# Kernel optimization log

Measured on AMD Instinct MI355X. Metric: run time of the kernel, lower is better.

Reference implementation:

```python
import jax, jax.numpy as jnp
from jax import lax
import numpy as np

B = 262144   # batch of independent series
K = 64       # forecast horizon (init k)
D_IN = 200   # Non_AR_net input dim (Linear(200,100))
H = 100      # hidden width


def setup_inputs() -> dict:
    key = jax.random.key(0)
    ks = jax.random.split(key, 10)
    f32 = jnp.float32
    x = jax.random.normal(ks[0], (B, D_IN), f32)
    last_mu = jax.random.normal(ks[1], (B,), f32)
    # last_sigma is the variance state; keep it strictly positive
    last_sigma = jax.random.uniform(ks[2], (B,), f32) + 0.5
    # MLP params (Kaiming-ish scale)
    W1 = jax.random.normal(ks[3], (D_IN, H), f32) / np.float32(np.sqrt(D_IN))
    b1 = jnp.zeros((H,), f32)
    W2 = jax.random.normal(ks[4], (H, H), f32) / np.float32(np.sqrt(H))
    b2 = jnp.zeros((H,), f32)
    W3 = jax.random.normal(ks[5], (H, K), f32) / np.float32(np.sqrt(H))
    b3 = jnp.zeros((K,), f32)
    return {
        "x": x, "last_mu": last_mu, "last_sigma": last_sigma,
        "alpha_mu": jnp.asarray(0.1, f32), "alpha_sigma": jnp.asarray(0.1, f32),
        "beta_mu": jnp.asarray(0.9, f32), "beta_sigma": jnp.asarray(0.85, f32),
        "omega_mu": jnp.asarray(0.0, f32), "omega_sigma": jnp.asarray(0.05, f32),
        "nu": jnp.asarray(5.0, f32), "norm_strength": jnp.asarray(1.0, f32),
        "W1": W1, "b1": b1, "W2": W2, "b2": b2, "W3": W3, "b3": b3,
    }


def _mlp(x, W1, b1, W2, b2, W3, b3):
    h = jax.nn.relu(x @ W1 + b1)
    h = jax.nn.relu(h @ W2 + b2)
    return h @ W3 + b3  # [B, K]


def _ar_gas(deep_preds, last_mu, last_sigma, a_mu, a_s, b_mu, b_s, o_mu, o_s, nu, ns):
    """Student-t score-driven (GAS) k-step recurrence, vectorized over batch.
    deep_preds: [B, K]; state mu, sigma2: [B]."""
    w = 1.0 + 1.0 / nu

    def step(carry, y):  # y: [B]
        mu, s2 = carry
        e = y - mu
        denom = 1.0 + e * e / (nu * s2)
        mu_new = o_mu + ns * a_mu * (w * e / denom) + b_mu * mu
        s2_new = o_s + ns * a_s * (w * e * e / denom - s2) + b_s * s2
        return (mu_new, s2_new), (mu_new, s2_new)

    (_, _), (mus, s2s) = lax.scan(step, (last_mu, last_sigma), deep_preds.T)
    return mus.T, jnp.sqrt(s2s.T)  # [B, K] each


def reference(x, last_mu, last_sigma, alpha_mu, alpha_sigma, beta_mu, beta_sigma,
              omega_mu, omega_sigma, nu, norm_strength,
              W1, b1, W2, b2, W3, b3):
    deep_preds = _mlp(x, W1, b1, W2, b2, W3, b3)            # [B, K]
    dp = lax.stop_gradient(deep_preds)                       # .detach() in torch
    mu_pred, sigma_pred = _ar_gas(dp, last_mu, last_sigma,
                                  alpha_mu, alpha_sigma, beta_mu, beta_sigma,
                                  omega_mu, omega_sigma, nu, norm_strength)
    return deep_preds * sigma_pred + mu_pred                 # [B, K]
```

## Files before the change

kernel.cpp:

```cpp
#include <hip/hip_runtime.h>
#include <hip/hip_bf16.h>

typedef short v8s __attribute__((ext_vector_type(8)));
typedef float v4f __attribute__((ext_vector_type(4)));

#define THREADS 256
#define BMROWS  128
#define W1F     0
#define W2F     49
#define W3F     77
#define W1LDS   28
#define SLABB   28672
#define LDS_TOTAL 78848

__device__ __forceinline__ unsigned short f2bf(float f) {
    union { __hip_bfloat16 h; unsigned short u; } c;
    c.h = __float2bfloat16(f);
    return c.u;
}
__device__ __forceinline__ unsigned pk2(float a, float b) {
    return (unsigned)f2bf(a) | ((unsigned)f2bf(b) << 16);
}
__device__ __forceinline__ v4f mfma16(v8s a, v8s b, v4f c) {
    return __builtin_amdgcn_mfma_f32_16x16x32_bf16(a, b, c, 0, 0, 0);
}
__device__ __forceinline__ v8s mkfrag(float4 a, float4 b) {
    union { unsigned u[4]; v8s s; } t;
    t.u[0] = pk2(a.x, a.y); t.u[1] = pk2(a.z, a.w);
    t.u[2] = pk2(b.x, b.y); t.u[3] = pk2(b.z, b.w);
    return t.s;
}
__device__ __forceinline__ void gload_lds16(const void* g, void* l) {
    __builtin_amdgcn_global_load_lds(
        (const __attribute__((address_space(1))) void*)g,
        (__attribute__((address_space(3))) void*)l, 16, 0, 0);
}

__global__ void prep_weights(const float* __restrict__ W1,
                             const float* __restrict__ W2,
                             const float* __restrict__ W3,
                             uint4* __restrict__ wf) {
    const int bid = blockIdx.x, l = threadIdx.x;
    const float* W; int K, N, KC, base, f;
    if (bid < 49)      { W = W1; K = 200; N = 100; KC = 7; base = W1F * 64; f = bid; }
    else if (bid < 77) { W = W2; K = 100; N = 100; KC = 4; base = W2F * 64; f = bid - 49; }
    else               { W = W3; K = 100; N = 64;  KC = 4; base = W3F * 64; f = bid - 77; }
    const int kc = f % KC;
    const int n  = (f / KC) * 16 + (l & 15);
    unsigned u[4];
    #pragma unroll
    for (int p = 0; p < 4; ++p) {
        const int k0 = kc * 32 + (l >> 4) * 8 + p * 2;
        const float a = (k0     < K && n < N) ? W[(size_t)k0 * N + n]       : 0.f;
        const float b = (k0 + 1 < K && n < N) ? W[(size_t)(k0 + 1) * N + n] : 0.f;
        u[p] = pk2(a, b);
    }
    wf[base + f * 64 + l] = make_uint4(u[0], u[1], u[2], u[3]);
}

__device__ __forceinline__ int sladdr(int wid, int row, int byte) {
    return SLABB + (wid << 13) + (row << 8) +
           ((((byte >> 4) ^ row) & 15) << 4) + (byte & 15);
}

__global__ __launch_bounds__(THREADS, 2)
void ar_gas_v12(const float* __restrict__ x,
                const float* __restrict__ last_mu,
                const float* __restrict__ last_sigma,
                const float* __restrict__ p_amu, const float* __restrict__ p_as,
                const float* __restrict__ p_bmu, const float* __restrict__ p_bs,
                const float* __restrict__ p_omu, const float* __restrict__ p_os,
                const float* __restrict__ p_nu,  const float* __restrict__ p_ns,
                const float* __restrict__ b1, const float* __restrict__ b2,
                const float* __restrict__ b3,
                const uint4* __restrict__ wf,
                float* __restrict__ out)
{
    extern __shared__ __align__(16) unsigned char L[];
    const int tid  = threadIdx.x;
    const int lane = tid & 63;
    const int wid  = tid >> 6;
    const int l15  = lane & 15;
    const int l4   = lane >> 4;
    const int blk  = blockIdx.x;

    const size_t gw = (size_t)blk * BMROWS + (size_t)wid * 32;
    const float* xp0 = x + (gw + l15) * 200;
    const float* xp1 = x + (gw + 16 + l15) * 200;

    const float mu_init = last_mu[gw + (lane & 31)];
    const float s2_init = last_sigma[gw + (lane & 31)];

#define XLOAD(d0, d1, xp, kk)                                           \
    { int kb = (kk) * 32 + l4 * 8;                                      \
      kb = (kb + 8 <= 200) ? kb : 168;                                  \
      d0 = *(const float4*)((xp) + kb);                                 \
      d1 = *(const float4*)((xp) + kb + 4); }

    float4 c0a, c0b, c1a, c1b;
    XLOAD(c0a, c0b, xp0, 0);
    XLOAD(c1a, c1b, xp1, 0);

    float bv[7];
    #pragma unroll
    for (int nt = 0; nt < 7; ++nt) {
        const int c = nt * 16 + l15;
        bv[nt] = (c < 100) ? b1[c] : 0.f;
    }

    for (int s = wid; s < 77; s += 4) {
        const int src = (s < 28) ? (W2F + s) : (W1F + s - 28);
        gload_lds16(wf + src * 64 + lane, L + s * 1024);
    }
    __syncthreads();

#define FRAG(slot) (*(const uint4*)(&L[(slot) * 1024 + lane * 16]))

    v4f acc[2][7];
    #pragma unroll
    for (int mt = 0; mt < 2; ++mt)
        #pragma unroll
        for (int nt = 0; nt < 7; ++nt) acc[mt][nt] = (v4f){0.f, 0.f, 0.f, 0.f};

    #pragma unroll
    for (int kc = 0; kc < 7; ++kc) {
        uint4 bu[7];
        #pragma unroll
        for (int nt = 0; nt < 7; ++nt) bu[nt] = FRAG(W1LDS + nt * 7 + kc);
        const v8s af0 = mkfrag(c0a, c0b);
        const v8s af1 = mkfrag(c1a, c1b);
        if (kc < 6) {
            XLOAD(c0a, c0b, xp0, kc + 1);
            XLOAD(c1a, c1b, xp1, kc + 1);
        }
        #pragma unroll
        for (int nt = 0; nt < 7; ++nt) {
            const v8s bf = *(const v8s*)&bu[nt];
            acc[0][nt] = mfma16(af0, bf, acc[0][nt]);
            acc[1][nt] = mfma16(af1, bf, acc[1][nt]);
        }
    }
#undef XLOAD

    __syncthreads();

    #pragma unroll
    for (int mt = 0; mt < 2; ++mt)
        #pragma unroll
        for (int nt = 0; nt < 7; ++nt) {
            #pragma unroll
            for (int r = 0; r < 4; ++r) {
                const int row = mt * 16 + l4 * 4 + r;
                const int c   = nt * 16 + l15;
                const float v = fmaxf(acc[mt][nt][r] + bv[nt], 0.f);
                *(unsigned short*)(&L[sladdr(wid, row, c * 2)]) = f2bf(v);
            }
        }
    *(uint4*)(&L[sladdr(wid, lane >> 1, 224 + (lane & 1) * 16)]) =
        make_uint4(0, 0, 0, 0);

    float bv2[7];
    #pragma unroll
    for (int nt = 0; nt < 7; ++nt) {
        const int c = nt * 16 + l15;
        bv2[nt] = (c < 100) ? b2[c] : 0.f;
    }
    v4f acc2[2][7];
    #pragma unroll
    for (int mt = 0; mt < 2; ++mt)
        #pragma unroll
        for (int nt = 0; nt < 7; ++nt) acc2[mt][nt] = (v4f){0.f, 0.f, 0.f, 0.f};

    #pragma unroll
    for (int kc = 0; kc < 4; ++kc) {
        uint4 bu[7];
        #pragma unroll
        for (int nt = 0; nt < 7; ++nt) bu[nt] = FRAG(nt * 4 + kc);
        uint4 t0 = *(const uint4*)(&L[sladdr(wid, l15,      kc * 64 + l4 * 16)]);
        uint4 t1 = *(const uint4*)(&L[sladdr(wid, 16 + l15, kc * 64 + l4 * 16)]);
        const v8s af0 = *(v8s*)&t0;
        const v8s af1 = *(v8s*)&t1;
        #pragma unroll
        for (int nt = 0; nt < 7; ++nt) {
            const v8s bf = *(const v8s*)&bu[nt];
            acc2[0][nt] = mfma16(af0, bf, acc2[0][nt]);
            acc2[1][nt] = mfma16(af1, bf, acc2[1][nt]);
        }
    }

    __syncthreads();

    for (int s = wid; s < 16; s += 4)
        gload_lds16(wf + (W3F + s) * 64 + lane, L + s * 1024);

    #pragma unroll
    for (int mt = 0; mt < 2; ++mt)
        #pragma unroll
        for (int nt = 0; nt < 7; ++nt) {
            #pragma unroll
            for (int r = 0; r < 4; ++r) {
                const int row = mt * 16 + l4 * 4 + r;
                const int c   = nt * 16 + l15;
                const float v = fmaxf(acc2[mt][nt][r] + bv2[nt], 0.f);
                *(unsigned short*)(&L[sladdr(wid, row, c * 2)]) = f2bf(v);
            }
        }

    __syncthreads();

    float bv3[4];
    #pragma unroll
    for (int nt = 0; nt < 4; ++nt) bv3[nt] = b3[nt * 16 + l15];
    v4f acc3[2][4];
    #pragma unroll
    for (int mt = 0; mt < 2; ++mt)
        #pragma unroll
        for (int nt = 0; nt < 4; ++nt) acc3[mt][nt] = (v4f){0.f, 0.f, 0.f, 0.f};

    #pragma unroll
    for (int kc = 0; kc < 4; ++kc) {
        uint4 bu[4];
        #pragma unroll
        for (int nt = 0; nt < 4; ++nt) bu[nt] = FRAG(nt * 4 + kc);
        uint4 t0 = *(const uint4*)(&L[sladdr(wid, l15,      kc * 64 + l4 * 16)]);
        uint4 t1 = *(const uint4*)(&L[sladdr(wid, 16 + l15, kc * 64 + l4 * 16)]);
        const v8s af0 = *(v8s*)&t0;
        const v8s af1 = *(v8s*)&t1;
        #pragma unroll
        for (int nt = 0; nt < 4; ++nt) {
            const v8s bf = *(const v8s*)&bu[nt];
            acc3[0][nt] = mfma16(af0, bf, acc3[0][nt]);
            acc3[1][nt] = mfma16(af1, bf, acc3[1][nt]);
        }
    }
#undef FRAG

    #pragma unroll
    for (int mt = 0; mt < 2; ++mt)
        #pragma unroll
        for (int nt = 0; nt < 4; ++nt) {
            #pragma unroll
            for (int r = 0; r < 4; ++r) {
                const int row = mt * 16 + l4 * 4 + r;
                const int c   = nt * 16 + l15;
                *(float*)(&L[sladdr(wid, row, c * 4)]) = acc3[mt][nt][r] + bv3[nt];
            }
        }

    if (lane < 32) {
        float mu = mu_init;
        float s2 = s2_init;
        const float anu = *p_nu,  ans = *p_ns;
        const float aMu = *p_amu, aSg = *p_as;
        const float bMu = *p_bmu, bSg = *p_bs;
        const float oMu = *p_omu, oSg = *p_os;
        const float w   = 1.f + __builtin_amdgcn_rcpf(anu);
        const float cmu = ans * aMu * w;
        const float cs  = ans * aSg * w;
        const float bs2 = bSg - ans * aSg;

#define GAS_STEP(Y, O)                                                  \
        {   const float e    = (Y) - mu;                                \
            const float nus2 = anu * s2;                                \
            const float den  = fmaf(e, e, nus2);                        \
            const float r0   = __builtin_amdgcn_rcpf(den);              \
            const float p    = e * nus2 * r0;                           \
            mu = fmaf(cmu, p, fmaf(bMu, mu, oMu));                      \
            s2 = fmaf(cs, e * p, fmaf(bs2, s2, oSg));                   \
            (O) = fmaf((Y), __builtin_amdgcn_sqrtf(s2), mu); }

        #pragma unroll
        for (int q = 0; q < 16; ++q) {
            float4 d = *(float4*)(&L[sladdr(wid, lane, q * 16)]);
            float o0, o1, o2, o3;
            GAS_STEP(d.x, o0); GAS_STEP(d.y, o1);
            GAS_STEP(d.z, o2); GAS_STEP(d.w, o3);
            *(float4*)(&L[sladdr(wid, lane, q * 16)]) = make_float4(o0, o1, o2, o3);
        }
#undef GAS_STEP
    }

    #pragma unroll
    for (int i = 0; i < 8; ++i) {
        const int fi  = i * 64 + lane;
        const int row = fi >> 4, q = fi & 15;
        float4 v = *(float4*)(&L[sladdr(wid, row, q * 16)]);
        ((float4*)out)[gw * 16 + fi] = v;
    }
}

extern "C" void kernel_launch(void* const* d_in, const int* in_sizes, int n_in,
                              void* d_out, int out_size, void* d_ws, size_t ws_size,
                              hipStream_t stream) {
    const float* x          = (const float*)d_in[0];
    const float* last_mu    = (const float*)d_in[1];
    const float* last_sigma = (const float*)d_in[2];
    const float* amu        = (const float*)d_in[3];
    const float* asig       = (const float*)d_in[4];
    const float* bmu        = (const float*)d_in[5];
    const float* bsig       = (const float*)d_in[6];
    const float* omu        = (const float*)d_in[7];
    const float* osig       = (const float*)d_in[8];
    const float* nu         = (const float*)d_in[9];
    const float* ns         = (const float*)d_in[10];
    const float* W1         = (const float*)d_in[11];
    const float* b1         = (const float*)d_in[12];
    const float* W2         = (const float*)d_in[13];
    const float* b2         = (const float*)d_in[14];
    const float* W3         = (const float*)d_in[15];
    const float* b3         = (const float*)d_in[16];
    float* out = (float*)d_out;

    uint4* wf = (uint4*)d_ws;
    prep_weights<<<93, 64, 0, stream>>>(W1, W2, W3, wf);

    hipFuncSetAttribute((const void*)ar_gas_v12,
                        hipFuncAttributeMaxDynamicSharedMemorySize, LDS_TOTAL);

    const int B = in_sizes[1];
    dim3 grid(B / BMROWS), block(THREADS);
    ar_gas_v12<<<grid, block, LDS_TOTAL, stream>>>(
        x, last_mu, last_sigma,
        amu, asig, bmu, bsig, omu, osig, nu, ns,
        b1, b2, b3, wf, out);
}
```

Before: 92.42 us.

## Make kernel persistent with resident weights and cross-tile x prefetch

Replaces the one-tile-per-block launch with a fixed grid of 256 blocks of 512 threads that each loop over four 256-row tiles. All three layers' weight fragments stay in LDS for the whole kernel, so the per-block reload and the mid-kernel W3 swap go away. The next tile's x is prefetched into registers while the GAS recurrence runs. LDS use grows to about 160KB per block, so likely one block per CU, and batch size and grid are now hardcoded.

```diff
diff --git a/kernel.cpp b/kernel.cpp
--- a/kernel.cpp
+++ b/kernel.cpp
@@ -4,14 +4,14 @@
 typedef short v8s __attribute__((ext_vector_type(8)));
 typedef float v4f __attribute__((ext_vector_type(4)));
 
-#define THREADS 256
-#define BMROWS  128
+#define THREADS 512
+#define TILE_ROWS 256
+#define NBLOCKS 256
 #define W1F     0
 #define W2F     49
 #define W3F     77
-#define W1LDS   28
-#define SLABB   28672
-#define LDS_TOTAL 78848
+#define SLABB   95232
+#define LDS_TOTAL (95232 + 8 * 8192)
 
 __device__ __forceinline__ unsigned short f2bf(float f) {
     union { __hip_bfloat16 h; unsigned short u; } c;
@@ -64,7 +64,7 @@
 }
 
 __global__ __launch_bounds__(THREADS, 2)
-void ar_gas_v12(const float* __restrict__ x,
+void ar_gas_v13(const float* __restrict__ x,
                 const float* __restrict__ last_mu,
                 const float* __restrict__ last_sigma,
                 const float* __restrict__ p_amu, const float* __restrict__ p_as,
@@ -84,12 +84,23 @@
     const int l4   = lane >> 4;
     const int blk  = blockIdx.x;
 
-    const size_t gw = (size_t)blk * BMROWS + (size_t)wid * 32;
-    const float* xp0 = x + (gw + l15) * 200;
-    const float* xp1 = x + (gw + 16 + l15) * 200;
-
-    const float mu_init = last_mu[gw + (lane & 31)];
-    const float s2_init = last_sigma[gw + (lane & 31)];
+    const float anu = *p_nu,  ans = *p_ns;
+    const float aMu = *p_amu, aSg = *p_as;
+    const float bMu = *p_bmu, bSg = *p_bs;
+    const float oMu = *p_omu, oSg = *p_os;
+    const float wS  = 1.f + __builtin_amdgcn_rcpf(anu);
+    const float cmu = ans * aMu * wS;
+    const float cs  = ans * aSg * wS;
+    const float bs2 = bSg - ans * aSg;
+    float bv1[7], bv2[7], bv3[4];
+    #pragma unroll
+    for (int nt = 0; nt < 7; ++nt) {
+        const int c = nt * 16 + l15;
+        bv1[nt] = (c < 100) ? b1[c] : 0.f;
+        bv2[nt] = (c < 100) ? b2[c] : 0.f;
+    }
+    #pragma unroll
+    for (int nt = 0; nt < 4; ++nt) bv3[nt] = b3[nt * 16 + l15];
 
 #define XLOAD(d0, d1, xp, kk)                                           \
     { int kb = (kk) * 32 + l4 * 8;                                      \
@@ -97,196 +108,186 @@
       d0 = *(const float4*)((xp) + kb);                                 \
       d1 = *(const float4*)((xp) + kb + 4); }
 
-    float4 c0a, c0b, c1a, c1b;
-    XLOAD(c0a, c0b, xp0, 0);
-    XLOAD(c1a, c1b, xp1, 0);
-
-    float bv[7];
-    #pragma unroll
-    for (int nt = 0; nt < 7; ++nt) {
-        const int c = nt * 16 + l15;
-        bv[nt] = (c < 100) ? b1[c] : 0.f;
+    float4 xv[3][2][2];
+    size_t gw = (size_t)blk * TILE_ROWS + (size_t)wid * 32;
+    {
+        const float* xp0 = x + (gw + l15) * 200;
+        const float* xp1 = xp0 + 16 * 200;
+        #pragma unroll
+        for (int c = 0; c < 3; ++c) {
+            XLOAD(xv[c][0][0], xv[c][0][1], xp0, c);
+            XLOAD(xv[c][1][0], xv[c][1][1], xp1, c);
+        }
     }
 
-    for (int s = wid; s < 77; s += 4) {
-        const int src = (s < 28) ? (W2F + s) : (W1F + s - 28);
-        gload_lds16(wf + src * 64 + lane, L + s * 1024);
-    }
+    for (int s = wid; s < 93; s += 8)
+        gload_lds16(wf + s * 64 + lane, L + s * 1024);
     __syncthreads();
 
 #define FRAG(slot) (*(const uint4*)(&L[(slot) * 1024 + lane * 16]))
 
-    v4f acc[2][7];
-    #pragma unroll
-    for (int mt = 0; mt < 2; ++mt)
-        #pragma unroll
-        for (int nt = 0; nt < 7; ++nt) acc[mt][nt] = (v4f){0.f, 0.f, 0.f, 0.f};
-
-    #pragma unroll
-    for (int kc = 0; kc < 7; ++kc) {
-        uint4 bu[7];
-        #pragma unroll
-        for (int nt = 0; nt < 7; ++nt) bu[nt] = FRAG(W1LDS + nt * 7 + kc);
-        const v8s af0 = mkfrag(c0a, c0b);
-        const v8s af1 = mkfrag(c1a, c1b);
-        if (kc < 6) {
-            XLOAD(c0a, c0b, xp0, kc + 1);
-            XLOAD(c1a, c1b, xp1, kc + 1);
-        }
-        #pragma unroll
-        for (int nt = 0; nt < 7; ++nt) {
-            const v8s bf = *(const v8s*)&bu[nt];
-            acc[0][nt] = mfma16(af0, bf, acc[0][nt]);
-            acc[1][nt] = mfma16(af1, bf, acc[1][nt]);
-        }
-    }
-#undef XLOAD
-
-    __syncthreads();
-
-    #pragma unroll
-    for (int mt = 0; mt < 2; ++mt)
-        #pragma unroll
-        for (int nt = 0; nt < 7; ++nt) {
-            #pragma unroll
-            for (int r = 0; r < 4; ++r) {
-                const int row = mt * 16 + l4 * 4 + r;
-                const int c   = nt * 16 + l15;
-                const float v = fmaxf(acc[mt][nt][r] + bv[nt], 0.f);
-                *(unsigned short*)(&L[sladdr(wid, row, c * 2)]) = f2bf(v);
-            }
-        }
-    *(uint4*)(&L[sladdr(wid, lane >> 1, 224 + (lane & 1) * 16)]) =
-        make_uint4(0, 0, 0, 0);
-
-    float bv2[7];
-    #pragma unroll
-    for (int nt = 0; nt < 7; ++nt) {
-        const int c = nt * 16 + l15;
-        bv2[nt] = (c < 100) ? b2[c] : 0.f;
-    }
-    v4f acc2[2][7];
-    #pragma unroll
-    for (int mt = 0; mt < 2; ++mt)
-        #pragma unroll
-        for (int nt = 0; nt < 7; ++nt) acc2[mt][nt] = (v4f){0.f, 0.f, 0.f, 0.f};
-
-    #pragma unroll
-    for (int kc = 0; kc < 4; ++kc) {
-        uint4 bu[7];
-        #pragma unroll
-        for (int nt = 0; nt < 7; ++nt) bu[nt] = FRAG(nt * 4 + kc);
-        uint4 t0 = *(const uint4*)(&L[sladdr(wid, l15,      kc * 64 + l4 * 16)]);
-        uint4 t1 = *(const uint4*)(&L[sladdr(wid, 16 + l15, kc * 64 + l4 * 16)]);
-        const v8s af0 = *(v8s*)&t0;
-        const v8s af1 = *(v8s*)&t1;
-        #pragma unroll
-        for (int nt = 0; nt < 7; ++nt) {
-            const v8s bf = *(const v8s*)&bu[nt];
-            acc2[0][nt] = mfma16(af0, bf, acc2[0][nt]);
-            acc2[1][nt] = mfma16(af1, bf, acc2[1][nt]);
-        }
-    }
-
-    __syncthreads();
-
-    for (int s = wid; s < 16; s += 4)
-        gload_lds16(wf + (W3F + s) * 64 + lane, L + s * 1024);
-
-    #pragma unroll
-    for (int mt = 0; mt < 2; ++mt)
-        #pragma unroll
-        for (int nt = 0; nt < 7; ++nt) {
-            #pragma unroll
-            for (int r = 0; r < 4; ++r) {
-                const int row = mt * 16 + l4 * 4 + r;
-                const int c   = nt * 16 + l15;
-                const float v = fmaxf(acc2[mt][nt][r] + bv2[nt], 0.f);
-                *(unsigned short*)(&L[sladdr(wid, row, c * 2)]) = f2bf(v);
-            }
-        }
-
-    __syncthreads();
-
-    float bv3[4];
-    #pragma unroll
-    for (int nt = 0; nt < 4; ++nt) bv3[nt] = b3[nt * 16 + l15];
-    v4f acc3[2][4];
-    #pragma unroll
-    for (int mt = 0; mt < 2; ++mt)
-        #pragma unroll
-        for (int nt = 0; nt < 4; ++nt) acc3[mt][nt] = (v4f){0.f, 0.f, 0.f, 0.f};
-
-    #pragma unroll
-    for (int kc = 0; kc < 4; ++kc) {
-        uint4 bu[4];
-        #pragma unroll
-        for (int nt = 0; nt < 4; ++nt) bu[nt] = FRAG(nt * 4 + kc);
-        uint4 t0 = *(const uint4*)(&L[sladdr(wid, l15,      kc * 64 + l4 * 16)]);
-        uint4 t1 = *(const uint4*)(&L[sladdr(wid, 16 + l15, kc * 64 + l4 * 16)]);
-        const v8s af0 = *(v8s*)&t0;
-        const v8s af1 = *(v8s*)&t1;
-        #pragma unroll
-        for (int nt = 0; nt < 4; ++nt) {
-            const v8s bf = *(const v8s*)&bu[nt];
-            acc3[0][nt] = mfma16(af0, bf, acc3[0][nt]);
-            acc3[1][nt] = mfma16(af1, bf, acc3[1][nt]);
-        }
+    #pragma unroll 1
+    for (int t = 0; t < 4; ++t) {
+        const float* xp0 = x + (gw + l15) * 200;
+        const float* xp1 = xp0 + 16 * 200;
+
+        const float mu_init = last_mu[gw + (lane & 31)];
+        const float s2_init = last_sigma[gw + (lane & 31)];
+
+        v4f acc[2][7];
+        #pragma unroll
+        for (int mt = 0; mt < 2; ++mt)
+            #pragma unroll
+            for (int nt = 0; nt < 7; ++nt) acc[mt][nt] = (v4f){0.f,0.f,0.f,0.f};
+
+        #pragma unroll
+        for (int kc = 0; kc < 7; ++kc) {
+            uint4 bu[7];
+            #pragma unroll
+            for (int nt = 0; nt < 7; ++nt) bu[nt] = FRAG(W1F + nt * 7 + kc);
+            const v8s af0 = mkfrag(xv[kc % 3][0][0], xv[kc % 3][0][1]);
+            const v8s af1 = mkfrag(xv[kc % 3][1][0], xv[kc % 3][1][1]);
+            if (kc < 4) {
+                XLOAD(xv[kc % 3][0][0], xv[kc % 3][0][1], xp0, kc + 3);
+                XLOAD(xv[kc % 3][1][0], xv[kc % 3][1][1], xp1, kc + 3);
+            }
+            #pragma unroll
+            for (int nt = 0; nt < 7; ++nt) {
+                const v8s bf = *(const v8s*)&bu[nt];
+                acc[0][nt] = mfma16(af0, bf, acc[0][nt]);
+                acc[1][nt] = mfma16(af1, bf, acc[1][nt]);
+            }
+        }
+
+        #pragma unroll
+        for (int mt = 0; mt < 2; ++mt)
+            #pragma unroll
+            for (int nt = 0; nt < 7; ++nt) {
+                #pragma unroll
+                for (int r = 0; r < 4; ++r) {
+                    const int row = mt * 16 + l4 * 4 + r;
+                    const int c   = nt * 16 + l15;
+                    const float v = fmaxf(acc[mt][nt][r] + bv1[nt], 0.f);
+                    *(unsigned short*)(&L[sladdr(wid, row, c * 2)]) = f2bf(v);
+                }
+            }
+        *(uint4*)(&L[sladdr(wid, lane >> 1, 224 + (lane & 1) * 16)]) =
+            make_uint4(0, 0, 0, 0);
+
+        v4f acc2[2][7];
+        #pragma unroll
+        for (int mt = 0; mt < 2; ++mt)
+            #pragma unroll
+            for (int nt = 0; nt < 7; ++nt) acc2[mt][nt] = (v4f){0.f,0.f,0.f,0.f};
+        #pragma unroll
+        for (int kc = 0; kc < 4; ++kc) {
+            uint4 bu[7];
+            #pragma unroll
+            for (int nt = 0; nt < 7; ++nt) bu[nt] = FRAG(W2F + nt * 4 + kc);
+            uint4 t0 = *(const uint4*)(&L[sladdr(wid, l15,      kc*64 + l4*16)]);
+            uint4 t1 = *(const uint4*)(&L[sladdr(wid, 16 + l15, kc*64 + l4*16)]);
+            const v8s af0 = *(v8s*)&t0;
+            const v8s af1 = *(v8s*)&t1;
+            #pragma unroll
+            for (int nt = 0; nt < 7; ++nt) {
+                const v8s bf = *(const v8s*)&bu[nt];
+                acc2[0][nt] = mfma16(af0, bf, acc2[0][nt]);
+                acc2[1][nt] = mfma16(af1, bf, acc2[1][nt]);
+            }
+        }
+        #pragma unroll
+        for (int mt = 0; mt < 2; ++mt)
+            #pragma unroll
+            for (int nt = 0; nt < 7; ++nt) {
+                #pragma unroll
+                for (int r = 0; r < 4; ++r) {
+                    const int row = mt * 16 + l4 * 4 + r;
+                    const int c   = nt * 16 + l15;
+                    const float v = fmaxf(acc2[mt][nt][r] + bv2[nt], 0.f);
+                    *(unsigned short*)(&L[sladdr(wid, row, c * 2)]) = f2bf(v);
+                }
+            }
+
+        v4f acc3[2][4];
+        #pragma unroll
+        for (int mt = 0; mt < 2; ++mt)
+            #pragma unroll
+            for (int nt = 0; nt < 4; ++nt) acc3[mt][nt] = (v4f){0.f,0.f,0.f,0.f};
+        #pragma unroll
+        for (int kc = 0; kc < 4; ++kc) {
+            uint4 bu[4];
+            #pragma unroll
+            for (int nt = 0; nt < 4; ++nt) bu[nt] = FRAG(W3F + nt * 4 + kc);
+            uint4 t0 = *(const uint4*)(&L[sladdr(wid, l15,      kc*64 + l4*16)]);
+            uint4 t1 = *(const uint4*)(&L[sladdr(wid, 16 + l15, kc*64 + l4*16)]);
+            const v8s af0 = *(v8s*)&t0;
+            const v8s af1 = *(v8s*)&t1;
+            #pragma unroll
+            for (int nt = 0; nt < 4; ++nt) {
+                const v8s bf = *(const v8s*)&bu[nt];
+                acc3[0][nt] = mfma16(af0, bf, acc3[0][nt]);
+                acc3[1][nt] = mfma16(af1, bf, acc3[1][nt]);
+            }
+        }
+        #pragma unroll
+        for (int mt = 0; mt < 2; ++mt)
+            #pragma unroll
+            for (int nt = 0; nt < 4; ++nt) {
+                #pragma unroll
+                for (int r = 0; r < 4; ++r) {
+                    const int row = mt * 16 + l4 * 4 + r;
+                    const int c   = nt * 16 + l15;
+                    *(float*)(&L[sladdr(wid, row, c * 4)]) = acc3[mt][nt][r] + bv3[nt];
+                }
+            }
+
+        const size_t gw_next = gw + (size_t)NBLOCKS * TILE_ROWS;
+        if (t < 3) {
+            const float* np0 = x + (gw_next + l15) * 200;
+            const float* np1 = np0 + 16 * 200;
+            #pragma unroll
+            for (int c = 0; c < 3; ++c) {
+                XLOAD(xv[c][0][0], xv[c][0][1], np0, c);
+                XLOAD(xv[c][1][0], xv[c][1][1], np1, c);
+            }
+        }
+
+        if (lane < 32) {
+            float mu = mu_init;
+            float s2 = s2_init;
+#define GAS_STEP(Y, O)                                                  \
+            {   const float e    = (Y) - mu;                            \
+                const float nus2 = anu * s2;                            \
+                const float den  = fmaf(e, e, nus2);                    \
+                const float r0   = __builtin_amdgcn_rcpf(den);          \
+                const float p    = e * nus2 * r0;                       \
+                mu = fmaf(cmu, p, fmaf(bMu, mu, oMu));                  \
+                s2 = fmaf(cs, e * p, fmaf(bs2, s2, oSg));               \
+                (O) = fmaf((Y), __builtin_amdgcn_sqrtf(s2), mu); }
+            #pragma unroll
+            for (int q = 0; q < 16; ++q) {
+                float4 d = *(float4*)(&L[sladdr(wid, lane, q * 16)]);
+                float o0, o1, o2, o3;
+                GAS_STEP(d.x, o0); GAS_STEP(d.y, o1);
+                GAS_STEP(d.z, o2); GAS_STEP(d.w, o3);
+                *(float4*)(&L[sladdr(wid, lane, q * 16)]) =
+                    make_float4(o0, o1, o2, o3);
+            }
+#undef GAS_STEP
+        }
+
+        #pragma unroll
+        for (int i = 0; i < 8; ++i) {
+            const int fi  = i * 64 + lane;
+            const int row = fi >> 4, q = fi & 15;
+            float4 v = *(float4*)(&L[sladdr(wid, row, q * 16)]);
+            ((float4*)out)[gw * 16 + fi] = v;
+        }
+
+        gw = gw_next;
     }
 #undef FRAG
-
-    #pragma unroll
-    for (int mt = 0; mt < 2; ++mt)
-        #pragma unroll
-        for (int nt = 0; nt < 4; ++nt) {
-            #pragma unroll
-            for (int r = 0; r < 4; ++r) {
-                const int row = mt * 16 + l4 * 4 + r;
-                const int c   = nt * 16 + l15;
-                *(float*)(&L[sladdr(wid, row, c * 4)]) = acc3[mt][nt][r] + bv3[nt];
-            }
-        }
-
-    if (lane < 32) {
-        float mu = mu_init;
-        float s2 = s2_init;
-        const float anu = *p_nu,  ans = *p_ns;
-        const float aMu = *p_amu, aSg = *p_as;
-        const float bMu = *p_bmu, bSg = *p_bs;
-        const float oMu = *p_omu, oSg = *p_os;
-        const float w   = 1.f + __builtin_amdgcn_rcpf(anu);
-        const float cmu = ans * aMu * w;
-        const float cs  = ans * aSg * w;
-        const float bs2 = bSg - ans * aSg;
-
-#define GAS_STEP(Y, O)                                                  \
-        {   const float e    = (Y) - mu;                                \
-            const float nus2 = anu * s2;                                \
-            const float den  = fmaf(e, e, nus2);                        \
-            const float r0   = __builtin_amdgcn_rcpf(den);              \
-            const float p    = e * nus2 * r0;                           \
-            mu = fmaf(cmu, p, fmaf(bMu, mu, oMu));                      \
-            s2 = fmaf(cs, e * p, fmaf(bs2, s2, oSg));                   \
-            (O) = fmaf((Y), __builtin_amdgcn_sqrtf(s2), mu); }
-
-        #pragma unroll
-        for (int q = 0; q < 16; ++q) {
-            float4 d = *(float4*)(&L[sladdr(wid, lane, q * 16)]);
-            float o0, o1, o2, o3;
-            GAS_STEP(d.x, o0); GAS_STEP(d.y, o1);
-            GAS_STEP(d.z, o2); GAS_STEP(d.w, o3);
-            *(float4*)(&L[sladdr(wid, lane, q * 16)]) = make_float4(o0, o1, o2, o3);
-        }
-#undef GAS_STEP
-    }
-
-    #pragma unroll
-    for (int i = 0; i < 8; ++i) {
-        const int fi  = i * 64 + lane;
-        const int row = fi >> 4, q = fi & 15;
-        float4 v = *(float4*)(&L[sladdr(wid, row, q * 16)]);
-        ((float4*)out)[gw * 16 + fi] = v;
-    }
+#undef XLOAD
 }
 
 extern "C" void kernel_launch(void* const* d_in, const int* in_sizes, int n_in,
@@ -314,12 +315,11 @@
     uint4* wf = (uint4*)d_ws;
     prep_weights<<<93, 64, 0, stream>>>(W1, W2, W3, wf);
 
-    hipFuncSetAttribute((const void*)ar_gas_v12,
+    hipFuncSetAttribute((const void*)ar_gas_v13,
                         hipFuncAttributeMaxDynamicSharedMemorySize, LDS_TOTAL);
 
-    const int B = in_sizes[1];
-    dim3 grid(B / BMROWS), block(THREADS);
-    ar_gas_v12<<<grid, block, LDS_TOTAL, stream>>>(
+    dim3 grid(NBLOCKS), block(THREADS);
+    ar_gas_v13<<<grid, block, LDS_TOTAL, stream>>>(
         x, last_mu, last_sigma,
         amu, asig, bmu, bsig, omu, osig, nu, ns,
         b1, b2, b3, wf, out);
```

Result: slower. 128.1 us (+38.6%).
